# Optimization experiments

Hardware: AMD Instinct MI355X
Metric: run time of the kernel (lower is better)

The kernel has to match this reference:

```python
import jax, jax.numpy as jnp
import numpy as np

B, N, HIST, PRED = 32, 1500, 24, 24
OUT, FDIM = 1, 31
IN = OUT + FDIM          # 32 = chebconv in_dim
HID, GCN, K, E = 256, 256, 3, 24000


def setup_inputs() -> dict:
    key = jax.random.key(0)
    ks = jax.random.split(key, 8)
    x_hist = jax.random.normal(ks[0], (B, HIST, N, OUT), jnp.float32)
    features = jax.random.normal(ks[1], (B, HIST + PRED, N, FDIM), jnp.float32)
    edge_index = jax.random.randint(ks[2], (2, E), 0, N, dtype=jnp.int32)
    s_cheb = 1.0 / np.sqrt(IN)
    s_ih = 1.0 / np.sqrt(HID)
    W_cheb = jax.random.normal(ks[3], (K, IN, GCN), jnp.float32) * s_cheb
    b_cheb = jnp.zeros((GCN,), jnp.float32)
    W_ih = jax.random.normal(ks[4], (3 * HID, IN + GCN), jnp.float32) * s_ih
    b_ih = jnp.zeros((3 * HID,), jnp.float32)
    W_hh = jax.random.normal(ks[5], (3 * HID, HID), jnp.float32) * s_ih
    b_hh = jnp.zeros((3 * HID,), jnp.float32)
    W_fc = jax.random.normal(ks[6], (OUT, HID), jnp.float32) * s_ih
    b_fc = jnp.zeros((OUT,), jnp.float32)
    return dict(x_hist=x_hist, features=features, edge_index=edge_index,
                W_cheb=W_cheb, b_cheb=b_cheb, W_ih=W_ih, b_ih=b_ih,
                W_hh=W_hh, b_hh=b_hh, W_fc=W_fc, b_fc=b_fc)


def _edge_norm(edge_index):
    # sym-normalized Laplacian scaled by 2/lambda_max with lambda_max=2:
    # L_hat = -D^{-1/2} A D^{-1/2} (zero diagonal)
    src, dst = edge_index[0], edge_index[1]
    deg = jax.ops.segment_sum(jnp.ones((E,), jnp.float32), src, num_segments=N)
    dis = jnp.where(deg > 0, jax.lax.rsqrt(jnp.maximum(deg, 1.0)), 0.0)
    w = -(dis[src] * dis[dst])
    return src, dst, w


def _cheb(x, src, dst, w, W_cheb, b_cheb):
    # x: [B, N, D]; Chebyshev recursion Tx_k = 2 L_hat Tx_{k-1} - Tx_{k-2}
    def Lx(v):
        msg = v[:, src, :] * w[None, :, None]          # [B, E, D]
        return jnp.zeros_like(v).at[:, dst, :].add(msg)
    Tx0 = x
    out = jnp.einsum('bnd,df->bnf', Tx0, W_cheb[0])
    Tx1 = Lx(x)
    out = out + jnp.einsum('bnd,df->bnf', Tx1, W_cheb[1])
    for k in range(2, W_cheb.shape[0]):
        Tx2 = 2.0 * Lx(Tx1) - Tx0
        out = out + jnp.einsum('bnd,df->bnf', Tx2, W_cheb[k])
        Tx0, Tx1 = Tx1, Tx2
    return out + b_cheb


def _gru(x, h, W_ih, b_ih, W_hh, b_hh):
    # x: [B*N, IN+GCN], h: [B*N, HID]; torch.nn.GRUCell math
    gi = x @ W_ih.T + b_ih
    gh = h @ W_hh.T + b_hh
    i_r, i_z, i_n = jnp.split(gi, 3, axis=-1)
    h_r, h_z, h_n = jnp.split(gh, 3, axis=-1)
    r = jax.nn.sigmoid(i_r + h_r)
    z = jax.nn.sigmoid(i_z + h_z)
    n = jnp.tanh(i_n + r * h_n)
    return (1.0 - z) * n + z * h


def reference(x_hist, features, edge_index, W_cheb, b_cheb, W_ih, b_ih, W_hh, b_hh, W_fc, b_fc):
    src, dst, w = _edge_norm(edge_index)

    def step(h, x_t):
        g = jax.nn.sigmoid(_cheb(x_t, src, dst, w, W_cheb, b_cheb))   # [B,N,GCN]
        xg = jnp.concatenate([x_t, g], axis=-1).reshape(B * N, IN + GCN)
        return _gru(xg, h, W_ih, b_ih, W_hh, b_hh)

    # encoder: t = 1 .. hist_len-1, x_t = [x_hist[:,t-1], features[:,t]]
    xs = jnp.concatenate([x_hist[:, :HIST - 1], features[:, 1:HIST]], axis=-1)
    xs = jnp.moveaxis(xs, 1, 0)                                       # [HIST-1,B,N,IN]
    h0 = jnp.zeros((B * N, HID), x_hist.dtype)
    hn, _ = jax.lax.scan(lambda h, x_t: (step(h, x_t), None), h0, xs)

    feats_dec = jnp.moveaxis(features[:, HIST:], 1, 0)                # [PRED,B,N,FDIM]

    def dec_step(carry, f_t):
        h, x_prev = carry
        x_t = jnp.concatenate([x_prev, f_t], axis=-1)                 # [B,N,IN]
        h = step(h, x_t)
        x_new = h.reshape(B, N, HID) @ W_fc.T + b_fc                  # [B,N,OUT]
        return (h, x_new), x_new

    (_, _), ys = jax.lax.scan(dec_step, (hn, x_hist[:, -1]), feats_dec)
    return jnp.moveaxis(ys, 0, 1)                                     # [B,PRED,N,OUT]
```

## Files before the change

kernel.cpp:

```cpp
#include <hip/hip_runtime.h>
#include <hip/hip_bf16.h>
#include <math.h>

#define NB 32
#define NN 1500
#define NE 24000
#define HIST_L 24
#define PRED_L 24
#define FDIM 31
#define INUM 32
#define HID 256
#define ROWS (NB*NN)
#define XGW 320
#define CTXW 96
#define NRB 375

typedef float f32x4 __attribute__((ext_vector_type(4)));
typedef short bf16x8 __attribute__((ext_vector_type(8)));
typedef short bf16x4 __attribute__((ext_vector_type(4)));

__device__ __forceinline__ float sigf(float x){ return 1.0f/(1.0f+expf(-x)); }
__device__ __forceinline__ unsigned short f2b(float f){
    __hip_bfloat16 h = __float2bfloat16(f);
    return __builtin_bit_cast(unsigned short, h);
}
__device__ __forceinline__ float b2f(unsigned short u){
    unsigned int x = ((unsigned int)u) << 16;
    return __builtin_bit_cast(float, x);
}

#define AS1 __attribute__((address_space(1)))
#define AS3 __attribute__((address_space(3)))
__device__ __forceinline__ void gload16(const void* g, void* l){
    __builtin_amdgcn_global_load_lds((const AS1 unsigned int*)g, (AS3 unsigned int*)l, 16, 0, 0);
}

__global__ void k_count(const int* __restrict__ ei, int* deg, int* cnt){
    int e = blockIdx.x*blockDim.x + threadIdx.x;
    if (e < NE){ atomicAdd(&deg[ei[e]], 1); atomicAdd(&cnt[ei[NE+e]], 1); }
}

__global__ void k_prefix(const int* __restrict__ cnt, int* __restrict__ coff){
    int lane = threadIdx.x;
    const int CH = (NN + 63)/64;
    int s = 0;
    for (int i=0;i<CH;i++){ int n = lane*CH+i; if (n<NN) s += cnt[n]; }
    int incl = s;
    for (int off=1; off<64; off<<=1){ int v = __shfl_up(incl, off); if (lane>=off) incl += v; }
    int run = incl - s;
    for (int i=0;i<CH;i++){ int n = lane*CH+i; if (n<NN){ coff[n] = run; run += cnt[n]; } }
    if (lane==63) coff[NN] = run;
}

__global__ __launch_bounds__(256) void k_fillw(
    const int* __restrict__ ei, const int* __restrict__ deg,
    const int* __restrict__ coff, int* __restrict__ csrc, float* __restrict__ cw){
    int n = blockIdx.x*4 + (threadIdx.x >> 6);
    if (n >= NN) return;
    int lane = threadIdx.x & 63;
    int dn = deg[n];
    float disn = dn>0 ? rsqrtf((float)dn) : 0.0f;
    int pos = coff[n];
    for (int base=0; base<NE; base+=64){
        int e = base + lane;
        int d = ei[NE+e];
        bool m = (d == n);
        unsigned long long mask = __ballot(m);
        if (m){
            int rank = __popcll(mask & ((1ull<<lane)-1ull));
            int s = ei[e];
            int ds = deg[s];
            float diss = ds>0 ? rsqrtf((float)ds) : 0.0f;
            csrc[pos+rank] = s;
            cw[pos+rank] = -(diss*disn);
        }
        pos += __popcll(mask);
    }
}

__global__ void k_f2b(const float* __restrict__ src, unsigned short* __restrict__ dst, int n){
    int i = blockIdx.x*256 + threadIdx.x;
    if (i < n) dst[i] = f2b(src[i]);
}
__global__ void k_wihr(const float* __restrict__ W, unsigned short* __restrict__ Wr){
    int i = blockIdx.x*256 + threadIdx.x;
    if (i < 768*XGW){
        int r = i/XGW, c = i - r*XGW;
        Wr[i] = (c < INUM+HID) ? f2b(W[(size_t)r*(INUM+HID) + c]) : (unsigned short)0;
    }
}
__global__ void k_wctr(const float* __restrict__ Wc, unsigned short* __restrict__ W){
    int i = blockIdx.x*256 + threadIdx.x;
    if (i < 256*96){
        int j = i/96, k = i - j*96;
        W[i] = f2b(Wc[(size_t)k*256 + j]);
    }
}

__global__ void k_build_xt(const float* __restrict__ ch0, int bstride, int choff, int addb,
                           const float* __restrict__ bfc,
                           const float* __restrict__ feats, int tf,
                           float* __restrict__ xt, unsigned short* __restrict__ ctx,
                           unsigned short* __restrict__ xg){
    int idx = blockIdx.x*blockDim.x + threadIdx.x;
    if (idx >= ROWS*INUM) return;
    int r = idx >> 5, c = idx & 31;
    int b = r / NN, n = r - b*NN;
    float v;
    if (c == 0){ v = ch0[b*bstride + choff + n]; if (addb) v += bfc[0]; }
    else         v = feats[((size_t)(b*(HIST_L+PRED_L) + tf)*NN + n)*FDIM + (c-1)];
    xt[idx] = v;
    unsigned short bv = f2b(v);
    ctx[(size_t)r*CTXW + c] = bv;
    xg[(size_t)r*XGW + c] = bv;
}

__global__ void k_lx4(const float* __restrict__ vin, const int* __restrict__ coff,
                      const int* __restrict__ csrc, const float* __restrict__ cw,
                      const float* __restrict__ sub, float scale,
                      float* __restrict__ vout, unsigned short* __restrict__ ctxo){
    int idx = blockIdx.x*256 + threadIdx.x;
    if (idx >= ROWS*8) return;
    int r = idx >> 3, l8 = idx & 7;
    int b = r / NN, n = r - b*NN;
    int j0 = coff[n], j1 = coff[n+1];
    const float4* vb = (const float4*)(vin + (size_t)b*NN*INUM);
    float ax=0.f, ay=0.f, az=0.f, aw=0.f;
    for (int j=j0;j<j1;j++){
        float w = cw[j];
        float4 v = vb[csrc[j]*8 + l8];
        ax += w*v.x; ay += w*v.y; az += w*v.z; aw += w*v.w;
    }
    ax *= scale; ay *= scale; az *= scale; aw *= scale;
    if (sub){
        float4 s = ((const float4*)sub)[idx];
        ax -= s.x; ay -= s.y; az -= s.z; aw -= s.w;
    }
    if (vout){
        float4 o; o.x=ax; o.y=ay; o.z=az; o.w=aw;
        ((float4*)vout)[idx] = o;
    }
    bf16x4 ob;
    ob[0]=(short)f2b(ax); ob[1]=(short)f2b(ay); ob[2]=(short)f2b(az); ob[3]=(short)f2b(aw);
    *(bf16x4*)&ctxo[(size_t)r*CTXW + l8*4] = ob;
}

__global__ __launch_bounds__(256,2) void k_cheb3(
    const unsigned short* __restrict__ ctx, const unsigned short* __restrict__ Wctr,
    const float* __restrict__ bc, unsigned short* __restrict__ xg)
{
    __shared__ __align__(16) unsigned short A[128*104];
    __shared__ __align__(16) unsigned short B[256*104];
    const int tid = threadIdx.x, wid = tid>>6, lane = tid&63;
    const int wm = wid>>1, wn = wid&1;
    const int r0 = blockIdx.x*128;
    const int l15 = lane&15, lhi = lane>>4;

    #pragma unroll
    for (int i=0;i<6;i++){
        int idx = tid + i*256;
        int row = idx/12, c = idx - row*12;
        *(int4*)&A[row*104 + c*8] = *(const int4*)&ctx[(size_t)(r0+row)*96 + c*8];
    }
    #pragma unroll
    for (int i=0;i<12;i++){
        int idx = tid + i*256;
        int row = idx/12, c = idx - row*12;
        *(int4*)&B[row*104 + c*8] = *(const int4*)&Wctr[(size_t)row*96 + c*8];
    }
    __syncthreads();

    f32x4 acc[4][8] = {};
    #pragma unroll
    for (int ks=0; ks<3; ks++){
        bf16x8 a[4];
        #pragma unroll
        for (int mi=0;mi<4;mi++)
            a[mi] = *(const bf16x8*)&A[(wm*64+mi*16+l15)*104 + ks*32 + lhi*8];
        #pragma unroll
        for (int ni=0;ni<8;ni++){
            bf16x8 b = *(const bf16x8*)&B[(wn*128+ni*16+l15)*104 + ks*32 + lhi*8];
            #pragma unroll
            for (int mi=0;mi<4;mi++)
                acc[mi][ni] = __builtin_amdgcn_mfma_f32_16x16x32_bf16(a[mi], b, acc[mi][ni],0,0,0);
        }
    }
    #pragma unroll
    for (int ni=0;ni<8;ni++){
        int col = wn*128 + ni*16 + l15;
        float bcv = bc[col];
        #pragma unroll
        for (int mi=0;mi<4;mi++){
            #pragma unroll
            for (int v=0;v<4;v++){
                size_t row = r0 + wm*64 + mi*16 + lhi*4 + v;
                xg[row*XGW + 32 + col] = f2b(sigf(acc[mi][ni][v] + bcv));
            }
        }
    }
}

__device__ __forceinline__ void gtile64(const unsigned short* Ap, const unsigned short* Bp,
    int wm, int wn, int l15, int q0, int q1,
    f32x4 (&ar)[4][2], f32x4 (&az)[4][2], f32x4 (&a3)[4][2])
{
    bf16x8 a[4][2];
    #pragma unroll
    for (int mi=0;mi<4;mi++){
        int rb = (wm*64 + mi*16 + l15)*64;
        a[mi][0] = *(const bf16x8*)&Ap[rb + q0];
        a[mi][1] = *(const bf16x8*)&Ap[rb + q1];
    }
    #pragma unroll
    for (int slab=0; slab<3; slab++){
        bf16x8 b[2][2];
        #pragma unroll
        for (int ni=0; ni<2; ni++){
            int cb = (slab*64 + wn*32 + ni*16 + l15)*64;
            b[ni][0] = *(const bf16x8*)&Bp[cb + q0];
            b[ni][1] = *(const bf16x8*)&Bp[cb + q1];
        }
        f32x4 (&acc)[4][2] = (slab==0)?ar:((slab==1)?az:a3);
        #pragma unroll
        for (int kh=0; kh<2; kh++)
            #pragma unroll
            for (int mi=0; mi<4; mi++)
                #pragma unroll
                for (int ni=0; ni<2; ni++)
                    acc[mi][ni] = __builtin_amdgcn_mfma_f32_16x16x32_bf16(a[mi][kh], b[ni][kh], acc[mi][ni],0,0,0);
    }
}

__global__ __launch_bounds__(256,2) void k_gru4(
    const unsigned short* __restrict__ xg, const unsigned short* __restrict__ hbin,
    const unsigned short* __restrict__ Wihr, const unsigned short* __restrict__ Whhr,
    const float* __restrict__ bih, const float* __restrict__ bhh,
    unsigned short* __restrict__ hbout,
    const float* __restrict__ Wfc, float* __restrict__ outp, int p)
{
    __shared__ __align__(16) unsigned short As[2][128*64];
    __shared__ __align__(16) unsigned short Bs[2][192*64];
    const int bi = blockIdx.x;
    const int xc = bi & 7, t = bi >> 3;
    const int R = xc + 8*(t>>2);
    if (R >= NRB) return;
    const int r0 = R*128, j0 = (t&3)*64;

    const int tid = threadIdx.x, wid = tid>>6, lane = tid&63;
    const int wm = wid>>1, wn = wid&1;
    const int l15 = lane&15, lhi = lane>>4, x7 = l15&7;
    const int q0 = (lhi^x7)*8, q1 = q0^32;
    const int swz = ((lane&7)^(lane>>3))*16;
    const int lr = lane>>3;

    f32x4 ar[4][2]={}, az[4][2]={}, ain[4][2]={}, ahn[4][2]={};

    auto stageA = [&](int ks, int bs){
        char* Ld = (char*)&As[bs][0] + wid*4096;
        const char* src; size_t stride;
        if (ks < 5){ src = (const char*)xg   + (size_t)r0*640 + (size_t)ks*128     + (size_t)lr*640 + swz; stride = 640; }
        else       { src = (const char*)hbin + (size_t)r0*512 + (size_t)(ks-5)*128 + (size_t)lr*512 + swz; stride = 512; }
        #pragma unroll
        for (int i=0;i<4;i++)
            gload16(src + (size_t)(wid*32 + i*8)*stride, Ld + i*1024);
    };
    auto stageB = [&](int ks, int bs){
        const char* src; size_t stride; int kb;
        if (ks < 5){ src = (const char*)Wihr; stride = 640; kb = ks; }
        else       { src = (const char*)Whhr; stride = 512; kb = ks-5; }
        src += (size_t)kb*128 + (size_t)lr*stride + swz;
        #pragma unroll
        for (int i=0;i<6;i++){
            int j = wid*6 + i; int slab = j>>3; int c0 = (j&7)*8;
            gload16(src + (size_t)(slab*256 + j0 + c0)*stride, (char*)&Bs[bs][0] + j*1024);
        }
    };

    stageA(0,0); stageB(0,0);
    __syncthreads();
    for (int ks=0; ks<5; ks++){
        int cur = ks&1;
        { stageA(ks+1, cur^1); stageB(ks+1, cur^1); }
        gtile64(&As[cur][0], &Bs[cur][0], wm, wn, l15, q0, q1, ar, az, ain);
        __syncthreads();
    }
    for (int ks=5; ks<9; ks++){
        int cur = ks&1;
        if (ks<8){ stageA(ks+1, cur^1); stageB(ks+1, cur^1); }
        gtile64(&As[cur][0], &Bs[cur][0], wm, wn, l15, q0, q1, ar, az, ahn);
        __syncthreads();
    }
    float fcp[4][4] = {};
    float wf[2];
    if (p >= 0){
        wf[0] = Wfc[j0 + wn*32 + l15];
        wf[1] = Wfc[j0 + wn*32 + 16 + l15];
    }
    #pragma unroll
    for (int ni=0; ni<2; ni++){
        int col = j0 + wn*32 + ni*16 + l15;
        float br = bih[col]       + bhh[col];
        float bz = bih[col+HID]   + bhh[col+HID];
        float bi = bih[col+2*HID];
        float bh = bhh[col+2*HID];
        #pragma unroll
        for (int mi=0; mi<4; mi++){
            #pragma unroll
            for (int v=0; v<4; v++){
                size_t row = r0 + wm*64 + mi*16 + lhi*4 + v;
                float r  = sigf(ar[mi][ni][v] + br);
                float z  = sigf(az[mi][ni][v] + bz);
                float nn = tanhf(ain[mi][ni][v] + bi + r*(ahn[mi][ni][v] + bh));
                float ho = b2f(hbin[row*HID + col]);
                float hv = (1.f - z)*nn + z*ho;
                hbout[row*HID + col] = f2b(hv);
                if (p >= 0) fcp[mi][v] += hv * wf[ni];
            }
        }
    }
    if (p >= 0){
        #pragma unroll
        for (int mi=0; mi<4; mi++){
            #pragma unroll
            for (int v=0; v<4; v++){
                float s = fcp[mi][v];
                s += __shfl_xor(s, 1);
                s += __shfl_xor(s, 2);
                s += __shfl_xor(s, 4);
                s += __shfl_xor(s, 8);
                if (l15 == 0){
                    int row = r0 + wm*64 + mi*16 + lhi*4 + v;
                    int bb = row / NN, n = row - bb*NN;
                    atomicAdd(&outp[(size_t)(bb*PRED_L + p)*NN + n], s);
                }
            }
        }
    }
}

extern "C" void kernel_launch(void* const* d_in, const int* in_sizes, int n_in,
                              void* d_out, int out_size, void* d_ws, size_t ws_size,
                              hipStream_t stream){
    const float* x_hist = (const float*)d_in[0];
    const float* feats  = (const float*)d_in[1];
    const int*   ei     = (const int*)d_in[2];
    const float* Wc     = (const float*)d_in[3];
    const float* bc     = (const float*)d_in[4];
    const float* Wih    = (const float*)d_in[5];
    const float* bih    = (const float*)d_in[6];
    const float* Whh    = (const float*)d_in[7];
    const float* bhh    = (const float*)d_in[8];
    const float* Wfc    = (const float*)d_in[9];
    const float* bfc    = (const float*)d_in[10];
    float* out = (float*)d_out;

    char* wsp = (char*)d_ws;
    size_t off = 0;
    auto alloc = [&](size_t bytes)->char*{
        char* p = wsp + off; off = (off + bytes + 255) & ~(size_t)255; return p;
    };
    int*   deg  = (int*)  alloc(NN*4);
    int*   cnt  = (int*)  alloc(NN*4);
    int*   coff = (int*)  alloc((NN+1)*4);
    int*   csrc = (int*)  alloc(NE*4);
    float* cw   = (float*)alloc(NE*4);
    float* xt   = (float*)alloc((size_t)ROWS*INUM*4);
    float* T1   = (float*)alloc((size_t)ROWS*INUM*4);
    unsigned short* ctx = (unsigned short*)alloc((size_t)ROWS*CTXW*2);
    unsigned short* xgb = (unsigned short*)alloc((size_t)ROWS*XGW*2);
    unsigned short* hbA = (unsigned short*)alloc((size_t)ROWS*HID*2);
    unsigned short* hbB = (unsigned short*)alloc((size_t)ROWS*HID*2);
    unsigned short* Wihr = (unsigned short*)alloc((size_t)768*XGW*2);
    unsigned short* Whhr = (unsigned short*)alloc((size_t)768*HID*2);
    unsigned short* Wctr = (unsigned short*)alloc((size_t)256*CTXW*2);

    hipMemsetAsync(deg, 0, NN*4, stream);
    hipMemsetAsync(cnt, 0, NN*4, stream);
    hipMemsetAsync(hbA, 0, (size_t)ROWS*HID*2, stream);
    hipMemsetAsync(xgb, 0, (size_t)ROWS*XGW*2, stream);
    hipMemsetAsync(out, 0, (size_t)out_size*4, stream);

    k_count<<<(NE+255)/256,256,0,stream>>>(ei, deg, cnt);
    k_prefix<<<1,64,0,stream>>>(cnt, coff);
    k_fillw<<<NRB,256,0,stream>>>(ei, deg, coff, csrc, cw);

    { int n = 768*XGW; k_wihr<<<(n+255)/256,256,0,stream>>>(Wih, Wihr); }
    { int n = 768*HID; k_f2b<<<(n+255)/256,256,0,stream>>>(Whh, Whhr, n); }
    { int n = 256*CTXW; k_wctr<<<(n+255)/256,256,0,stream>>>(Wc, Wctr); }

    unsigned short* hbin = hbA; unsigned short* hbout = hbB;
    const int gruGrid = 1504;
    const int chebGrid = NRB;
    const int NT  = (ROWS*INUM+255)/256;
    const int NT8 = (ROWS*8+255)/256;

    auto step = [&](const float* ch0, int bstride, int choff, int addb, int tf, int p){
        k_build_xt<<<NT,256,0,stream>>>(ch0, bstride, choff, addb, bfc, feats, tf, xt, ctx, xgb);
        k_lx4<<<NT8,256,0,stream>>>(xt, coff, csrc, cw, nullptr, 1.f, T1, ctx + 32);
        k_lx4<<<NT8,256,0,stream>>>(T1, coff, csrc, cw, xt, 2.f, nullptr, ctx + 64);
        k_cheb3<<<chebGrid,256,0,stream>>>(ctx, Wctr, bc, xgb);
        k_gru4<<<gruGrid,256,0,stream>>>(xgb, hbin, Wihr, Whhr, bih, bhh, hbout, Wfc, out, p);
        unsigned short* t = hbin; hbin = hbout; hbout = t;
    };

    for (int t=0;t<HIST_L-1;t++)
        step(x_hist, HIST_L*NN, t*NN, 0, t+1, -1);
    for (int p=0;p<PRED_L;p++){
        if (p==0) step(x_hist, HIST_L*NN, (HIST_L-1)*NN, 0, HIST_L+p, p);
        else      step(out, PRED_L*NN, (p-1)*NN, 1, HIST_L+p, p);
    }
}
```

Measured before the change: 7.102 ms.

## Batch encoder Chebyshev stages across multiple timesteps per launch

In the encoder the graph-conv inputs do not depend on the hidden state, so the build, Laplacian and Chebyshev GEMM kernels now run for up to CH timesteps at once using a 2D grid or extra blocks. Only the GRU kernels stay sequential. This cuts launch count and fills more of the GPU on the smaller kernels. In exchange it needs more workspace per slice, and CH falls back to 1 if the workspace is too small.

```diff
diff --git a/kernel.cpp b/kernel.cpp
--- a/kernel.cpp
+++ b/kernel.cpp
@@ -97,13 +97,19 @@
     }
 }
 
-__global__ void k_build_xt(const float* __restrict__ ch0, int bstride, int choff, int addb,
-                           const float* __restrict__ bfc,
-                           const float* __restrict__ feats, int tf,
-                           float* __restrict__ xt, unsigned short* __restrict__ ctx,
-                           unsigned short* __restrict__ xg){
+__global__ void k_build(const float* __restrict__ ch0, int bstride, int choff0, int chstep, int addb,
+                        const float* __restrict__ bfc,
+                        const float* __restrict__ feats, int tf0,
+                        float* __restrict__ xt, unsigned short* __restrict__ ctx,
+                        unsigned short* __restrict__ xg){
+    int s = blockIdx.y;
     int idx = blockIdx.x*blockDim.x + threadIdx.x;
     if (idx >= ROWS*INUM) return;
+    xt  += (size_t)s*ROWS*INUM;
+    ctx += (size_t)s*ROWS*CTXW;
+    xg  += (size_t)s*ROWS*XGW;
+    int choff = choff0 + s*chstep;
+    int tf = tf0 + s;
     int r = idx >> 5, c = idx & 31;
     int b = r / NN, n = r - b*NN;
     float v;
@@ -119,8 +125,13 @@
                       const int* __restrict__ csrc, const float* __restrict__ cw,
                       const float* __restrict__ sub, float scale,
                       float* __restrict__ vout, unsigned short* __restrict__ ctxo){
+    int s = blockIdx.y;
     int idx = blockIdx.x*256 + threadIdx.x;
     if (idx >= ROWS*8) return;
+    vin += (size_t)s*ROWS*INUM;
+    if (sub)  sub  += (size_t)s*ROWS*INUM;
+    if (vout) vout += (size_t)s*ROWS*INUM;
+    ctxo += (size_t)s*ROWS*CTXW;
     int r = idx >> 3, l8 = idx & 7;
     int b = r / NN, n = r - b*NN;
     int j0 = coff[n], j1 = coff[n+1];
@@ -133,8 +144,8 @@
     }
     ax *= scale; ay *= scale; az *= scale; aw *= scale;
     if (sub){
-        float4 s = ((const float4*)sub)[idx];
-        ax -= s.x; ay -= s.y; az -= s.z; aw -= s.w;
+        float4 sv = ((const float4*)sub)[idx];
+        ax -= sv.x; ay -= sv.y; az -= sv.z; aw -= sv.w;
     }
     if (vout){
         float4 o; o.x=ax; o.y=ay; o.z=az; o.w=aw;
@@ -151,9 +162,13 @@
 {
     __shared__ __align__(16) unsigned short A[128*104];
     __shared__ __align__(16) unsigned short B[256*104];
+    const int bi = blockIdx.x;
+    const int s = bi / NRB, rb = bi - s*NRB;
+    ctx += (size_t)s*ROWS*CTXW;
+    xg  += (size_t)s*ROWS*XGW;
     const int tid = threadIdx.x, wid = tid>>6, lane = tid&63;
     const int wm = wid>>1, wn = wid&1;
-    const int r0 = blockIdx.x*128;
+    const int r0 = rb*128;
     const int l15 = lane&15, lhi = lane>>4;
 
     #pragma unroll
@@ -301,7 +316,7 @@
         int col = j0 + wn*32 + ni*16 + l15;
         float br = bih[col]       + bhh[col];
         float bz = bih[col+HID]   + bhh[col+HID];
-        float bi = bih[col+2*HID];
+        float bi2 = bih[col+2*HID];
         float bh = bhh[col+2*HID];
         #pragma unroll
         for (int mi=0; mi<4; mi++){
@@ -310,7 +325,7 @@
                 size_t row = r0 + wm*64 + mi*16 + lhi*4 + v;
                 float r  = sigf(ar[mi][ni][v] + br);
                 float z  = sigf(az[mi][ni][v] + bz);
-                float nn = tanhf(ain[mi][ni][v] + bi + r*(ahn[mi][ni][v] + bh));
+                float nn = tanhf(ain[mi][ni][v] + bi2 + r*(ahn[mi][ni][v] + bh));
                 float ho = b2f(hbin[row*HID + col]);
                 float hv = (1.f - z)*nn + z*ho;
                 hbout[row*HID + col] = f2b(hv);
@@ -364,20 +379,26 @@
     int*   coff = (int*)  alloc((NN+1)*4);
     int*   csrc = (int*)  alloc(NE*4);
     float* cw   = (float*)alloc(NE*4);
-    float* xt   = (float*)alloc((size_t)ROWS*INUM*4);
-    float* T1   = (float*)alloc((size_t)ROWS*INUM*4);
-    unsigned short* ctx = (unsigned short*)alloc((size_t)ROWS*CTXW*2);
-    unsigned short* xgb = (unsigned short*)alloc((size_t)ROWS*XGW*2);
     unsigned short* hbA = (unsigned short*)alloc((size_t)ROWS*HID*2);
     unsigned short* hbB = (unsigned short*)alloc((size_t)ROWS*HID*2);
     unsigned short* Wihr = (unsigned short*)alloc((size_t)768*XGW*2);
     unsigned short* Whhr = (unsigned short*)alloc((size_t)768*HID*2);
     unsigned short* Wctr = (unsigned short*)alloc((size_t)256*CTXW*2);
 
+    const size_t perSlice = (size_t)ROWS*INUM*4*2 + (size_t)ROWS*CTXW*2 + (size_t)ROWS*XGW*2 + 4*256;
+    int CH = 1;
+    for (int c : {8,6,4,2}){
+        if (off + (size_t)c*perSlice + (1<<20) <= ws_size){ CH = c; break; }
+    }
+    float* xt_b = (float*)alloc((size_t)CH*ROWS*INUM*4);
+    float* T1_b = (float*)alloc((size_t)CH*ROWS*INUM*4);
+    unsigned short* ctx_b = (unsigned short*)alloc((size_t)CH*ROWS*CTXW*2);
+    unsigned short* xg_b  = (unsigned short*)alloc((size_t)CH*ROWS*XGW*2);
+
     hipMemsetAsync(deg, 0, NN*4, stream);
     hipMemsetAsync(cnt, 0, NN*4, stream);
     hipMemsetAsync(hbA, 0, (size_t)ROWS*HID*2, stream);
-    hipMemsetAsync(xgb, 0, (size_t)ROWS*XGW*2, stream);
+    hipMemsetAsync(xg_b, 0, (size_t)CH*ROWS*XGW*2, stream);
     hipMemsetAsync(out, 0, (size_t)out_size*4, stream);
 
     k_count<<<(NE+255)/256,256,0,stream>>>(ei, deg, cnt);
@@ -390,23 +411,29 @@
 
     unsigned short* hbin = hbA; unsigned short* hbout = hbB;
     const int gruGrid = 1504;
-    const int chebGrid = NRB;
     const int NT  = (ROWS*INUM+255)/256;
     const int NT8 = (ROWS*8+255)/256;
 
-    auto step = [&](const float* ch0, int bstride, int choff, int addb, int tf, int p){
-        k_build_xt<<<NT,256,0,stream>>>(ch0, bstride, choff, addb, bfc, feats, tf, xt, ctx, xgb);
-        k_lx4<<<NT8,256,0,stream>>>(xt, coff, csrc, cw, nullptr, 1.f, T1, ctx + 32);
-        k_lx4<<<NT8,256,0,stream>>>(T1, coff, csrc, cw, xt, 2.f, nullptr, ctx + 64);
-        k_cheb3<<<chebGrid,256,0,stream>>>(ctx, Wctr, bc, xgb);
-        k_gru4<<<gruGrid,256,0,stream>>>(xgb, hbin, Wihr, Whhr, bih, bhh, hbout, Wfc, out, p);
-        unsigned short* t = hbin; hbin = hbout; hbout = t;
-    };
-
-    for (int t=0;t<HIST_L-1;t++)
-        step(x_hist, HIST_L*NN, t*NN, 0, t+1, -1);
+    for (int t0=0; t0<HIST_L-1; t0+=CH){
+        int nc = HIST_L-1-t0; if (nc > CH) nc = CH;
+        dim3 gb(NT, nc), gl(NT8, nc);
+        k_build<<<gb,256,0,stream>>>(x_hist, HIST_L*NN, t0*NN, NN, 0, bfc, feats, t0+1, xt_b, ctx_b, xg_b);
+        k_lx4<<<gl,256,0,stream>>>(xt_b, coff, csrc, cw, nullptr, 1.f, T1_b, ctx_b + 32);
+        k_lx4<<<gl,256,0,stream>>>(T1_b, coff, csrc, cw, xt_b, 2.f, nullptr, ctx_b + 64);
+        k_cheb3<<<NRB*nc,256,0,stream>>>(ctx_b, Wctr, bc, xg_b);
+        for (int s=0; s<nc; s++){
+            k_gru4<<<gruGrid,256,0,stream>>>(xg_b + (size_t)s*ROWS*XGW, hbin, Wihr, Whhr, bih, bhh, hbout, Wfc, out, -1);
+            unsigned short* tmp = hbin; hbin = hbout; hbout = tmp;
+        }
+    }
     for (int p=0;p<PRED_L;p++){
-        if (p==0) step(x_hist, HIST_L*NN, (HIST_L-1)*NN, 0, HIST_L+p, p);
-        else      step(out, PRED_L*NN, (p-1)*NN, 1, HIST_L+p, p);
-    }
-}
+        dim3 gb(NT,1), gl(NT8,1);
+        if (p==0) k_build<<<gb,256,0,stream>>>(x_hist, HIST_L*NN, (HIST_L-1)*NN, 0, 0, bfc, feats, HIST_L+p, xt_b, ctx_b, xg_b);
+        else      k_build<<<gb,256,0,stream>>>(out, PRED_L*NN, (p-1)*NN, 0, 1, bfc, feats, HIST_L+p, xt_b, ctx_b, xg_b);
+        k_lx4<<<gl,256,0,stream>>>(xt_b, coff, csrc, cw, nullptr, 1.f, T1_b, ctx_b + 32);
+        k_lx4<<<gl,256,0,stream>>>(T1_b, coff, csrc, cw, xt_b, 2.f, nullptr, ctx_b + 64);
+        k_cheb3<<<NRB,256,0,stream>>>(ctx_b, Wctr, bc, xg_b);
+        k_gru4<<<gruGrid,256,0,stream>>>(xg_b, hbin, Wihr, Whhr, bih, bhh, hbout, Wfc, out, p);
+        unsigned short* tmp = hbin; hbin = hbout; hbout = tmp;
+    }
+}
```

Measured after the change: 6.875 ms (median of 2 runs). -3.2%, faster.
